# Optimization experiments

Hardware: AMD Instinct MI355X
Metric: run time of the kernel (lower is better)

Reference implementation:

```python
import jax, jax.numpy as jnp
import numpy as np

D = 1024      # input_dim = clip_model.text_projection.shape[1]
P = D // 8    # pre_dim1 == pre_dim2 == 128
B, NS, NT, C = 4096, 8192, 8192, 1000
EPS = 1e-5
SCALE = 0.1
BETA_S = 1.0
BETA_T = 1.0


def setup_inputs() -> dict:
    key = jax.random.key(0)
    ks = jax.random.split(key, 24)
    rn = lambda k, shp, s=0.02: jax.random.normal(k, shp, dtype=jnp.float32) * s
    inp = {
        "Ft": jax.random.normal(ks[0], (C, D), dtype=jnp.float32),
        "Fv": jax.random.normal(ks[1], (B, D), dtype=jnp.float32),
        "Fvs_bank": jax.random.normal(ks[2], (NS, D), dtype=jnp.float32),
        "Fvt_bank": jax.random.normal(ks[3], (NT, D), dtype=jnp.float32),
        # pre_project: Linear(D->P), BN(P), ReLU, Linear(P->P), BN(P), ReLU, Linear(P->3D)
        "W1": rn(ks[4], (P, D)), "b1": jnp.zeros((P,), jnp.float32),
        "g1": jnp.ones((P,), jnp.float32), "be1": jnp.zeros((P,), jnp.float32),
        "m1": jnp.zeros((P,), jnp.float32), "v1": jnp.ones((P,), jnp.float32),
        "W2": rn(ks[5], (P, P)), "b2": jnp.zeros((P,), jnp.float32),
        "g2": jnp.ones((P,), jnp.float32), "be2": jnp.zeros((P,), jnp.float32),
        "m2": jnp.zeros((P,), jnp.float32), "v2": jnp.ones((P,), jnp.float32),
        "W3": rn(ks[6], (3 * D, P)), "b3": jnp.zeros((3 * D,), jnp.float32),
        # post_project: Linear(D->D)
        "Wp": rn(ks[7], (D, D)), "bp": jnp.zeros((D,), jnp.float32),
        "logit_scale": jnp.asarray(np.log(1.0 / 0.07), dtype=jnp.float32),
    }
    return inp


def _pre_project(x, W1, b1, g1, be1, m1, v1, W2, b2, g2, be2, m2, v2, W3, b3):
    # Linear -> BatchNorm1d (eval: running stats) -> ReLU, twice, then Linear to 3*D
    h = x @ W1.T + b1
    h = jax.nn.relu((h - m1) * jax.lax.rsqrt(v1 + EPS) * g1 + be1)
    h = h @ W2.T + b2
    h = jax.nn.relu((h - m2) * jax.lax.rsqrt(v2 + EPS) * g2 + be2)
    return h @ W3.T + b3  # (n, 3*D)


def _qkv(o):
    # einops 'b (d k) -> k b d' with k=3: interleaved split along last dim
    o = o.reshape(o.shape[0], D, 3)
    return o[..., 0], o[..., 1], o[..., 2]


def reference(Ft, Fv, Fvs_bank, Fvt_bank, W1, b1, g1, be1, m1, v1,
              W2, b2, g2, be2, m2, v2, W3, b3, Wp, bp, logit_scale):
    pre = lambda x: _pre_project(x, W1, b1, g1, be1, m1, v1,
                                 W2, b2, g2, be2, m2, v2, W3, b3)
    q_fv, _, _ = _qkv(pre(Fv))
    _, k_fvs, v_fvs = _qkv(pre(Fvs_bank))
    _, k_fvt, v_fvt = _qkv(pre(Fvt_bank))

    As = jax.nn.softmax(SCALE * (q_fv @ k_fvs.T), axis=-1)  # (B, NS)
    At = jax.nn.softmax(SCALE * (q_fv @ k_fvt.T), axis=-1)  # (B, NT)

    Fsa = Fv + (As @ v_fvs) @ Wp.T + bp
    Fta = Fv + (At @ v_fvt) @ Wp.T + bp
    Fsa = Fsa / jnp.linalg.norm(Fsa, axis=-1, keepdims=True)
    Fta = Fta / jnp.linalg.norm(Fta, axis=-1, keepdims=True)

    ls = jnp.exp(logit_scale)
    logits = BETA_S * ls * (Fsa @ Ft.T) + BETA_T * ls * (Fta @ Ft.T)
    return logits  # (B, C)
```

## Files before the change

kernel.cpp:

```cpp
#include <hip/hip_runtime.h>
#include <hip/hip_bf16.h>
#include <math.h>

#define D_DIM   1024
#define P_DIM   128
#define B_ROWS  4096
#define NBANK   8192
#define C_CLS   1000
#define EPS_BN  1e-5f
#define SCALE_S 0.1f
#define MTOT    20480
#define KVSEG   16
#define KCH     64
#define CHUNKS  (NBANK / KVSEG / KCH)

typedef __bf16 bf16x8 __attribute__((ext_vector_type(8)));
typedef float  f32x4  __attribute__((ext_vector_type(4)));
typedef __hip_bfloat16 bf;

__device__ __forceinline__ void load_lds16(const void* gp, void* lp) {
    __builtin_amdgcn_global_load_lds(
        (__attribute__((address_space(1))) void*)gp,
        (__attribute__((address_space(3))) void*)lp, 16, 0, 0);
}

__device__ __forceinline__ int4 pack8(float4 a, float4 b) {
    union { bf h[8]; int4 v; } u;
    u.h[0] = __float2bfloat16(a.x); u.h[1] = __float2bfloat16(a.y);
    u.h[2] = __float2bfloat16(a.z); u.h[3] = __float2bfloat16(a.w);
    u.h[4] = __float2bfloat16(b.x); u.h[5] = __float2bfloat16(b.y);
    u.h[6] = __float2bfloat16(b.z); u.h[7] = __float2bfloat16(b.w);
    return u.v;
}

__global__ __launch_bounds__(256)
void gemm_bf16(const bf* __restrict__ A, const bf* __restrict__ B,
               int M, int N, int K, int lda, int ldb,
               int kchunks, int fx, int fy, int epi,
               float* __restrict__ Cf, bf* __restrict__ Cb,
               const float* __restrict__ bias, const float* __restrict__ biasm,
               const float* __restrict__ bng, const float* __restrict__ bnb,
               const float* __restrict__ bnm, const float* __restrict__ bnv,
               const float* __restrict__ addsrc, const float* __restrict__ lsp,
               int ldc)
{
    __shared__ __align__(16) short ldsS[8192];
    short* lsA = ldsS;
    short* lsB = ldsS + 4096;

    const int tid  = threadIdx.x;
    const int wave = tid >> 6;
    const int lane = tid & 63;
    const int wm   = wave >> 1;
    const int wn   = wave & 1;
    const int r16  = lane & 15;
    const int quad = lane >> 4;

    const int gx = gridDim.x, gy = gridDim.y;
    const int l   = blockIdx.y * gx + blockIdx.x;
    const int xcd = l & 7;
    const int i0  = l >> 3;
    const int sx  = gx / fx, sy = gy / fy;
    const int bx  = (xcd % fx) * sx + (i0 % sx);
    const int by  = (xcd / fx) * sy + (i0 / sx);
    const int bm0 = by * 128;
    const int bn0 = bx * 128;

    const int kper = K / kchunks;
    const int kbeg = blockIdx.z * kper;
    const int kend = kbeg + kper;

    f32x4 acc[4][4];
#pragma unroll
    for (int i = 0; i < 4; ++i)
#pragma unroll
        for (int j = 0; j < 4; ++j) acc[i][j] = (f32x4){0.f, 0.f, 0.f, 0.f};

    for (int k0 = kbeg; k0 < kend; k0 += 32) {
#pragma unroll
        for (int i = 0; i < 2; ++i) {
            const int s   = i * 256 + tid;
            const int row = s >> 2;
            const int cc  = (s & 3) * 8;
            const int lofs = (i * 256 + wave * 64) * 16;
            load_lds16(A + (size_t)(bm0 + row) * lda + k0 + cc, (char*)lsA + lofs);
            load_lds16(B + (size_t)(bn0 + row) * ldb + k0 + cc, (char*)lsB + lofs);
        }
        __syncthreads();

        bf16x8 af[4], bfr[4];
#pragma unroll
        for (int i = 0; i < 4; ++i)
            af[i] = *(const bf16x8*)(lsA + (wm * 64 + i * 16 + r16) * 32 + quad * 8);
#pragma unroll
        for (int j = 0; j < 4; ++j)
            bfr[j] = *(const bf16x8*)(lsB + (wn * 64 + j * 16 + r16) * 32 + quad * 8);
#pragma unroll
        for (int i = 0; i < 4; ++i)
#pragma unroll
            for (int j = 0; j < 4; ++j)
                acc[i][j] = __builtin_amdgcn_mfma_f32_16x16x32_bf16(
                    af[i], bfr[j], acc[i][j], 0, 0, 0);
        __syncthreads();
    }

    if (epi == 3 || epi == 4) {
        const float lsv = (epi == 4) ? expf(*lsp) : 1.0f;
#pragma unroll
        for (int i = 0; i < 4; ++i) {
            const int gmb = bm0 + wm * 64 + i * 16 + quad * 4;
#pragma unroll
            for (int j = 0; j < 4; ++j) {
                const int gn = bn0 + wn * 64 + j * 16 + r16;
#pragma unroll
                for (int r = 0; r < 4; ++r) {
                    const int gm = gmb + r;
                    float val = acc[i][j][r];
                    if (epi == 3) {
                        Cf[(size_t)gm * N + gn] =
                            val + bias[gn] + addsrc[(size_t)(gm & (ldc - 1)) * N + gn];
                    } else {
                        if (gn < ldc) Cf[(size_t)gm * ldc + gn] = val * lsv;
                    }
                }
            }
        }
        return;
    }

    bf* dst = Cb + (epi == 6 ? (size_t)blockIdx.z * M * N : 0);
    bf* my  = (bf*)(ldsS + wave * 2048);

#pragma unroll
    for (int half = 0; half < 2; ++half) {
#pragma unroll
        for (int i2 = 0; i2 < 2; ++i2) {
            const int i = half * 2 + i2;
            const int gmb = bm0 + wm * 64 + i * 16 + quad * 4;
#pragma unroll
            for (int j = 0; j < 4; ++j) {
                const int gn = bn0 + wn * 64 + j * 16 + r16;
#pragma unroll
                for (int r = 0; r < 4; ++r) {
                    float val = acc[i][j][r];
                    if (epi == 1) {
                        val += bias[gn];
                        val = (val - bnm[gn]) * rsqrtf(bnv[gn] + EPS_BN) * bng[gn] + bnb[gn];
                        val = fmaxf(val, 0.f);
                    } else {
                        if (bias)  val += bias[gn];
                        if (biasm) val += biasm[gmb + r];
                    }
                    my[(i2 * 16 + quad * 4 + r) * 64 + j * 16 + r16] =
                        __float2bfloat16(val);
                }
            }
        }
#pragma unroll
        for (int it = 0; it < 4; ++it) {
            const int chunk = it * 64 + lane;
            const int lrow  = chunk >> 3;
            const int lcol  = (chunk & 7) * 8;
            const int grow  = bm0 + wm * 64 + half * 32 + lrow;
            const int gcol  = bn0 + wn * 64 + lcol;
            int4 v = *(const int4*)(my + lrow * 64 + lcol);
            *(int4*)(dst + (size_t)grow * N + gcol) = v;
        }
    }
}

__global__ __launch_bounds__(512)
void attn_fused(const bf* __restrict__ qt,
                const bf* __restrict__ h2bank,
                const bf* __restrict__ h2T,
                const float* __restrict__ beta,
                bf* __restrict__ Ypart,
                float* __restrict__ rsP)
{
    __shared__ __align__(16) short lds[24576];
    short* lsK = lds;
    short* lsV = lds + 8192;
    short* lsS = lds + 16384;

    const int tid  = threadIdx.x;
    const int wave = tid >> 6;
    const int lane = tid & 63;
    const int r16  = lane & 15;
    const int quad = lane >> 4;

    const int qb   = blockIdx.x >> 5;
    const int side = (blockIdx.x >> 4) & 1;
    const int seg  = blockIdx.x & 15;
    const int part = side * KVSEG + seg;
    const int nseg0 = seg * (NBANK / KVSEG);
    const bf* kbase = h2bank + (size_t)side * NBANK * P_DIM;
    const int ncol0 = side * NBANK;

    const bf* qrow = qt + (size_t)(qb * 128 + wave * 16 + r16) * P_DIM;
    bf16x8 qreg[4];
#pragma unroll
    for (int ks = 0; ks < 4; ++ks)
        qreg[ks] = *(const bf16x8*)(qrow + (ks * 4 + quad) * 8);

    f32x4 yacc[8];
    float rsacc[4] = {0.f, 0.f, 0.f, 0.f};
#pragma unroll
    for (int j = 0; j < 8; ++j) yacc[j] = (f32x4){0.f, 0.f, 0.f, 0.f};

    for (int c = 0; c < CHUNKS; ++c) {
        const int kv0 = nseg0 + c * KCH;
        __syncthreads();
#pragma unroll
        for (int m = 0; m < 2; ++m) {
            const int s = m * 512 + tid;
            const int row = s >> 4, pcg = s & 15;
            const int lcg = pcg ^ (row & 15);
            load_lds16(kbase + (size_t)(kv0 + row) * P_DIM + lcg * 8,
                       (char*)lsK + (m * 512 + wave * 64) * 16);
        }
#pragma unroll
        for (int m = 0; m < 2; ++m) {
            const int s = m * 512 + tid;
            const int row = s >> 3, pcg = s & 7;
            const int lcg = pcg ^ (row & 7);
            load_lds16(h2T + (size_t)row * (2 * NBANK) + ncol0 + kv0 + lcg * 8,
                       (char*)lsV + (m * 512 + wave * 64) * 16);
        }
        __syncthreads();

        f32x4 sacc[4];
#pragma unroll
        for (int j = 0; j < 4; ++j) sacc[j] = (f32x4){0.f, 0.f, 0.f, 0.f};
#pragma unroll
        for (int ks = 0; ks < 4; ++ks) {
            bf16x8 bfr[4];
#pragma unroll
            for (int j = 0; j < 4; ++j) {
                const int kr = j * 16 + r16;
                bfr[j] = *(const bf16x8*)(lsK + kr * 128 +
                                          ((ks * 4 + quad) ^ (kr & 15)) * 8);
            }
#pragma unroll
            for (int j = 0; j < 4; ++j)
                sacc[j] = __builtin_amdgcn_mfma_f32_16x16x32_bf16(
                    qreg[ks], bfr[j], sacc[j], 0, 0, 0);
        }

#pragma unroll
        for (int j = 0; j < 4; ++j) {
            const int col = j * 16 + r16;
            const float bv = beta[(size_t)side * NBANK + kv0 + col];
            const int cg = col >> 3, cl = col & 7;
#pragma unroll
            for (int r = 0; r < 4; ++r) {
                const int row = wave * 16 + quad * 4 + r;
                float v = __expf(SCALE_S * (sacc[j][r] + bv));
                rsacc[r] += v;
                ((bf*)lsS)[row * 64 + ((cg ^ (row & 7)) << 3) + cl] =
                    __float2bfloat16(v);
            }
        }

#pragma unroll
        for (int ks = 0; ks < 2; ++ks) {
            const int sr = wave * 16 + r16;
            bf16x8 pa = *(const bf16x8*)(lsS + sr * 64 +
                                         ((ks * 4 + quad) ^ (sr & 7)) * 8);
            bf16x8 pb[8];
#pragma unroll
            for (int j = 0; j < 8; ++j) {
                const int vr = j * 16 + r16;
                pb[j] = *(const bf16x8*)(lsV + vr * 64 +
                                         ((ks * 4 + quad) ^ (vr & 7)) * 8);
            }
#pragma unroll
            for (int j = 0; j < 8; ++j)
                yacc[j] = __builtin_amdgcn_mfma_f32_16x16x32_bf16(
                    pa, pb[j], yacc[j], 0, 0, 0);
        }
    }

#pragma unroll
    for (int r = 0; r < 4; ++r) {
        float s = rsacc[r];
        s += __shfl_xor(s, 1, 64);
        s += __shfl_xor(s, 2, 64);
        s += __shfl_xor(s, 4, 64);
        s += __shfl_xor(s, 8, 64);
        rsacc[r] = s;
    }
    if (r16 == 0)
        *(float4*)(rsP + (size_t)part * B_ROWS + qb * 128 + wave * 16 + quad * 4) =
            (float4){rsacc[0], rsacc[1], rsacc[2], rsacc[3]};

    __syncthreads();
    bf* my = (bf*)lds + wave * 2048;
#pragma unroll
    for (int j = 0; j < 8; ++j)
#pragma unroll
        for (int r = 0; r < 4; ++r)
            my[(quad * 4 + r) * 128 + j * 16 + r16] =
                __float2bfloat16(yacc[j][r]);
    bf* dst = Ypart + (size_t)part * B_ROWS * P_DIM
                    + (size_t)(qb * 128 + wave * 16) * P_DIM;
#pragma unroll
    for (int it = 0; it < 4; ++it) {
        const int chunk = it * 64 + lane;
        const int lrow  = chunk >> 4;
        const int lcol  = (chunk & 15) * 8;
        *(int4*)(dst + (size_t)lrow * P_DIM + lcol) =
            *(const int4*)(my + lrow * 128 + lcol);
    }
}

#define PG0 10240
#define PG1 584
#define PG2 64
#define PG3 512
#define PG4 8
#define PG5 256

__global__ __launch_bounds__(256)
void prep(const float* __restrict__ Fv, const float* __restrict__ Fvs,
          const float* __restrict__ Fvt,
          const float* __restrict__ W1, const float* __restrict__ W2,
          const float* __restrict__ Wp,
          const float* __restrict__ W3, const float* __restrict__ b3,
          const float* __restrict__ bp, const float* __restrict__ Ft,
          bf* __restrict__ Xb, bf* __restrict__ W1b, bf* __restrict__ W2b,
          bf* __restrict__ Wpb,
          bf* __restrict__ Tq, bf* __restrict__ Tk, bf* __restrict__ Tv,
          bf* __restrict__ Ftb,
          float* __restrict__ vvecP, float* __restrict__ bvp)
{
    const int tid = threadIdx.x;
    int b = blockIdx.x;
    if (b < PG0) {
        int i = (b * 256 + tid) * 8;
        const int n0 = B_ROWS * D_DIM, n1 = n0 + NBANK * D_DIM;
        const float* src; int off;
        if (i < n0)      { src = Fv;  off = i; }
        else if (i < n1) { src = Fvs; off = i - n0; }
        else             { src = Fvt; off = i - n1; }
        float4 a = *(const float4*)(src + off);
        float4 c = *(const float4*)(src + off + 4);
        *(int4*)(Xb + i) = pack8(a, c);
        return;
    }
    if ((b -= PG0) < PG1) {
        int i = (b * 256 + tid) * 8;
        const int n1 = P_DIM * D_DIM, n2 = n1 + P_DIM * P_DIM;
        const float* src; bf* dst; int off;
        if (i < n1)      { src = W1; dst = W1b; off = i; }
        else if (i < n2) { src = W2; dst = W2b; off = i - n1; }
        else             { src = Wp; dst = Wpb; off = i - n2; }
        float4 a = *(const float4*)(src + off);
        float4 c = *(const float4*)(src + off + 4);
        *(int4*)(dst + off) = pack8(a, c);
        return;
    }
    if ((b -= PG1) < PG2) {
        int i = (b * 256 + tid) * 8;
        int p = i >> 10, d0 = i & 1023;
        union { bf h[8]; int4 v; } uq, uk, uv;
#pragma unroll
        for (int j = 0; j < 8; ++j) {
            const float* r = W3 + (size_t)3 * (d0 + j) * P_DIM + p;
            uq.h[j] = __float2bfloat16(r[0]);
            uk.h[j] = __float2bfloat16(r[P_DIM]);
            uv.h[j] = __float2bfloat16(r[2 * P_DIM]);
        }
        *(int4*)(Tq + i) = uq.v;
        *(int4*)(Tk + i) = uk.v;
        *(int4*)(Tv + i) = uv.v;
        return;
    }
    if ((b -= PG2) < PG3) {
        int i = (b * 256 + tid) * 8;
        int row = i >> 10, col = i & 1023;
        if (row < C_CLS) {
            float4 a = *(const float4*)(Ft + (size_t)row * D_DIM + col);
            float4 c = *(const float4*)(Ft + (size_t)row * D_DIM + col + 4);
            *(int4*)(Ftb + i) = pack8(a, c);
        } else {
            *(int4*)(Ftb + i) = (int4){0, 0, 0, 0};
        }
        return;
    }
    if ((b -= PG3) < PG4) {
        const int p = tid & 127, hf = tid >> 7;
        const int dbase = b * 128 + hf * 64;
        float s = 0.f;
        for (int dd = 0; dd < 64; ++dd) {
            const int d = dbase + dd;
            s = fmaf(b3[3 * d], W3[(size_t)(3 * d + 1) * P_DIM + p], s);
        }
        vvecP[(b * 2 + hf) * P_DIM + p] = s;
        return;
    }
    b -= PG4;
    const int wave = tid >> 6, lane = tid & 63;
    const int o = b * 4 + wave;
    const float* r = Wp + (size_t)o * D_DIM;
    float s = 0.f;
    for (int i = lane; i < D_DIM; i += 64) s = fmaf(r[i], b3[3 * i + 2], s);
    for (int off = 32; off > 0; off >>= 1) s += __shfl_down(s, off, 64);
    if (lane == 0) bvp[o] = s + bp[o];
}

__global__ __launch_bounds__(256)
void reduceWW(const bf* __restrict__ WqkP, const bf* __restrict__ WpvP,
              bf* __restrict__ Wqk, bf* __restrict__ Wpv)
{
    const int tid = threadIdx.x;
    if (blockIdx.x < 8) {
        int i = (blockIdx.x * 256 + tid) * 8;
        float s[8] = {};
        for (int z = 0; z < 8; ++z) {
            union { int4 v; bf h[8]; } u;
            u.v = *(const int4*)(WqkP + (size_t)z * 16384 + i);
#pragma unroll
            for (int e = 0; e < 8; ++e) s[e] += __bfloat162float(u.h[e]);
        }
        union { bf h[8]; int4 v; } o;
#pragma unroll
        for (int e = 0; e < 8; ++e) o.h[e] = __float2bfloat16(s[e]);
        *(int4*)(Wqk + i) = o.v;
    } else {
        int i = ((blockIdx.x - 8) * 256 + tid) * 8;
        float s[8] = {};
        for (int z = 0; z < 4; ++z) {
            union { int4 v; bf h[8]; } u;
            u.v = *(const int4*)(WpvP + (size_t)z * 131072 + i);
#pragma unroll
            for (int e = 0; e < 8; ++e) s[e] += __bfloat162float(u.h[e]);
        }
        union { bf h[8]; int4 v; } o;
#pragma unroll
        for (int e = 0; e < 8; ++e) o.h[e] = __float2bfloat16(s[e]);
        *(int4*)(Wpv + i) = o.v;
    }
}

__global__ __launch_bounds__(256)
void posth2(const bf* __restrict__ h2bank, const float* __restrict__ vvecP,
            float* __restrict__ beta, bf* __restrict__ h2T)
{
    __shared__ float vs[P_DIM];
    __shared__ bf t[64][136];
    const int tid = threadIdx.x;
    if (blockIdx.x < 64) {
        if (tid < P_DIM) {
            float s = 0.f;
#pragma unroll
            for (int z = 0; z < 16; ++z) s += vvecP[z * P_DIM + tid];
            vs[tid] = s;
        }
        __syncthreads();
        const int n = blockIdx.x * 256 + tid;
        const bf* r = h2bank + (size_t)n * P_DIM;
        float s = 0.f;
#pragma unroll
        for (int c = 0; c < P_DIM; c += 8) {
            union { int4 q; bf h[8]; } u;
            u.q = *(const int4*)(r + c);
#pragma unroll
            for (int e = 0; e < 8; ++e) s += __bfloat162float(u.h[e]) * vs[c + e];
        }
        beta[n] = s;
    } else {
        const size_t n0 = (size_t)(blockIdx.x - 64) * 64;
#pragma unroll
        for (int q = 0; q < 4; ++q) {
            int idx = (q * 256 + tid) * 8;
            int r = idx >> 7, c = idx & 127;
            *(int4*)&t[r][c] = *(const int4*)(h2bank + (n0 + r) * P_DIM + c);
        }
        __syncthreads();
        const int p  = tid >> 1;
        const int nb = (tid & 1) * 32;
#pragma unroll
        for (int q = 0; q < 4; ++q) {
            const int n = nb + q * 8;
            union { int4 v; bf h[8]; } u;
#pragma unroll
            for (int e = 0; e < 8; ++e) u.h[e] = t[n + e][p];
            *(int4*)(h2T + (size_t)p * (2 * NBANK) + n0 + n) = u.v;
        }
    }
}

__global__ __launch_bounds__(256)
void reduceY(const bf* __restrict__ parts, const float* __restrict__ rsP,
             bf* __restrict__ Yhat)
{
    int j = (blockIdx.x * 256 + threadIdx.x) * 8;
    const int s = j >> 19;
    const int qrow = (j >> 7) & (B_ROWS - 1);
    float rs = 0.f;
#pragma unroll
    for (int g = 0; g < KVSEG; ++g)
        rs += rsP[(size_t)(s * KVSEG + g) * B_ROWS + qrow];
    const bf* p = parts + (size_t)s * KVSEG * 524288 + (size_t)(j & 524287);
    float acc[8] = {};
    for (int z = 0; z < KVSEG; ++z) {
        union { int4 v; bf h[8]; } u;
        u.v = *(const int4*)(p + (size_t)z * 524288);
#pragma unroll
        for (int e = 0; e < 8; ++e) acc[e] += __bfloat162float(u.h[e]);
    }
    const float inv = 1.0f / rs;
    union { bf h[8]; int4 v; } o;
#pragma unroll
    for (int e = 0; e < 8; ++e) o.h[e] = __float2bfloat16(acc[e] * inv);
    *(int4*)(Yhat + j) = o.v;
}

__global__ __launch_bounds__(256)
void rownorm2b(const float* __restrict__ G, bf* __restrict__ out)
{
    __shared__ float red[16];
    const int tid = threadIdx.x;
    const float* ps = G + (size_t)blockIdx.x * D_DIM;
    const float* pt = ps + (size_t)B_ROWS * D_DIM;
    float4 a = *(const float4*)(ps + tid * 4);
    float4 c = *(const float4*)(pt + tid * 4);
    float sa = a.x * a.x + a.y * a.y + a.z * a.z + a.w * a.w;
    float sb = c.x * c.x + c.y * c.y + c.z * c.z + c.w * c.w;
    for (int s = 32; s > 0; s >>= 1) {
        sa += __shfl_down(sa, s, 64);
        sb += __shfl_down(sb, s, 64);
    }
    if ((tid & 63) == 0) { red[tid >> 6] = sa; red[8 + (tid >> 6)] = sb; }
    __syncthreads();
    if (tid == 0) {
        float ta = 0.f, tb = 0.f;
        for (int w = 0; w < 4; ++w) { ta += red[w]; tb += red[8 + w]; }
        red[4] = rsqrtf(ta); red[12] = rsqrtf(tb);
    }
    __syncthreads();
    const float ia = red[4], ib = red[12];
    union { bf h[4]; int2 v; } o;
    o.h[0] = __float2bfloat16(a.x * ia + c.x * ib);
    o.h[1] = __float2bfloat16(a.y * ia + c.y * ib);
    o.h[2] = __float2bfloat16(a.z * ia + c.z * ib);
    o.h[3] = __float2bfloat16(a.w * ia + c.w * ib);
    *(int2*)(out + (size_t)blockIdx.x * D_DIM + tid * 4) = o.v;
}

extern "C" void kernel_launch(void* const* d_in, const int* in_sizes, int n_in,
                              void* d_out, int out_size, void* d_ws, size_t ws_size,
                              hipStream_t stream)
{
    (void)in_sizes; (void)n_in; (void)out_size; (void)ws_size;

    const float* Ft  = (const float*)d_in[0];
    const float* Fv  = (const float*)d_in[1];
    const float* Fvs = (const float*)d_in[2];
    const float* Fvt = (const float*)d_in[3];
    const float* W1  = (const float*)d_in[4];
    const float* b1  = (const float*)d_in[5];
    const float* g1  = (const float*)d_in[6];
    const float* be1 = (const float*)d_in[7];
    const float* m1  = (const float*)d_in[8];
    const float* v1  = (const float*)d_in[9];
    const float* W2  = (const float*)d_in[10];
    const float* b2  = (const float*)d_in[11];
    const float* g2  = (const float*)d_in[12];
    const float* be2 = (const float*)d_in[13];
    const float* m2  = (const float*)d_in[14];
    const float* v2  = (const float*)d_in[15];
    const float* W3  = (const float*)d_in[16];
    const float* b3  = (const float*)d_in[17];
    const float* Wp  = (const float*)d_in[18];
    const float* bp  = (const float*)d_in[19];
    const float* ls  = (const float*)d_in[20];

    char* base = (char*)d_ws;
    size_t o = 0;
    auto take = [&](size_t s) { size_t r = o; o += (s + 255) & ~(size_t)255; return r; };

    bf* qtb   = (bf*)(base + take((size_t)B_ROWS * P_DIM * 2));
    bf* h2T   = (bf*)(base + take((size_t)P_DIM * 2 * NBANK * 2));
    bf* Yhat  = (bf*)(base + take((size_t)2 * B_ROWS * P_DIM * 2));
    bf* Wpb   = (bf*)(base + take((size_t)D_DIM * D_DIM * 2));
    bf* Ftb   = (bf*)(base + take((size_t)D_DIM * D_DIM * 2));
    bf* W3qT  = (bf*)(base + take((size_t)P_DIM * D_DIM * 2));
    bf* W3kT  = (bf*)(base + take((size_t)P_DIM * D_DIM * 2));
    bf* W3vT  = (bf*)(base + take((size_t)P_DIM * D_DIM * 2));
    bf* Wqk   = (bf*)(base + take((size_t)P_DIM * P_DIM * 2));
    bf* Wpvb  = (bf*)(base + take((size_t)D_DIM * P_DIM * 2));
    bf* W1b   = (bf*)(base + take((size_t)P_DIM * D_DIM * 2));
    bf* W2b   = (bf*)(base + take((size_t)P_DIM * P_DIM * 2));
    bf* h2b   = (bf*)(base + take((size_t)MTOT * P_DIM * 2));
    bf* WqkP  = (bf*)(base + take((size_t)8 * P_DIM * P_DIM * 2));
    bf* WpvP  = (bf*)(base + take((size_t)4 * D_DIM * P_DIM * 2));
    float* vvecP = (float*)(base + take((size_t)16 * P_DIM * 4));
    float* beta  = (float*)(base + take((size_t)2 * NBANK * 4));
    float* bvp   = (float*)(base + take(D_DIM * 4));
    float* rsP   = (float*)(base + take((size_t)2 * KVSEG * B_ROWS * 4));

    const size_t Dbase = o;
    bf* Xb    = (bf*)(base + Dbase);
    bf* h1b   = (bf*)(base + Dbase + (size_t)MTOT * D_DIM * 2);
    bf* Opart = (bf*)(base + Dbase + (size_t)48 * 1024 * 1024);
    float* G     = (float*)(base + Dbase);
    bf*    Fsumb = (bf*)(base + Dbase + (size_t)2 * B_ROWS * D_DIM * 4);

    auto gemm = [&](const bf* A, const bf* B, int M, int N, int K, int lda, int ldb,
                    int kch, int fx, int fy, int epi, float* Cf, bf* Cb,
                    const float* bias, const float* biasm,
                    const float* bg, const float* bb, const float* bm, const float* bv,
                    const float* addsrc, const float* lsp, int ldc) {
        gemm_bf16<<<dim3(N / 128, M / 128, kch), dim3(256), 0, stream>>>(
            A, B, M, N, K, lda, ldb, kch, fx, fy, epi, Cf, Cb, bias, biasm,
            bg, bb, bm, bv, addsrc, lsp, ldc);
    };

    prep<<<dim3(PG0 + PG1 + PG2 + PG3 + PG4 + PG5), dim3(256), 0, stream>>>(
        Fv, Fvs, Fvt, W1, W2, Wp, W3, b3, bp, Ft,
        Xb, W1b, W2b, Wpb, W3qT, W3kT, W3vT, Ftb, vvecP, bvp);

    gemm(W3kT, W3qT, P_DIM, P_DIM, D_DIM, D_DIM, D_DIM, 8, 1, 1, 6, nullptr, WqkP,
         nullptr, nullptr, nullptr, nullptr, nullptr, nullptr, nullptr, nullptr, 0);
    gemm(Wpb, W3vT, D_DIM, P_DIM, D_DIM, D_DIM, D_DIM, 4, 1, 8, 6, nullptr, WpvP,
         nullptr, nullptr, nullptr, nullptr, nullptr, nullptr, nullptr, nullptr, 0);
    reduceWW<<<dim3(72), dim3(256), 0, stream>>>(WqkP, WpvP, Wqk, Wpvb);

    gemm(Xb, W1b, MTOT, P_DIM, D_DIM, D_DIM, D_DIM, 1, 1, 8, 1, nullptr, h1b,
         b1, nullptr, g1, be1, m1, v1, nullptr, nullptr, 0);
    gemm(h1b, W2b, MTOT, P_DIM, P_DIM, P_DIM, P_DIM, 1, 1, 8, 1, nullptr, h2b,
         b2, nullptr, g2, be2, m2, v2, nullptr, nullptr, 0);
    gemm(h2b, Wqk, B_ROWS, P_DIM, P_DIM, P_DIM, P_DIM, 1, 1, 8, 5, nullptr, qtb,
         nullptr, nullptr, nullptr, nullptr, nullptr, nullptr, nullptr, nullptr, 0);
    posth2<<<dim3(320), dim3(256), 0, stream>>>(
        h2b + (size_t)B_ROWS * P_DIM, vvecP, beta, h2T);

    attn_fused<<<dim3(2 * KVSEG * (B_ROWS / 128)), dim3(512), 0, stream>>>(
        qtb, h2b + (size_t)B_ROWS * P_DIM, h2T, beta, Opart, rsP);
    reduceY<<<dim3(2 * B_ROWS * P_DIM / 2048), dim3(256), 0, stream>>>(
        Opart, rsP, Yhat);

    gemm(Yhat, Wpvb, 2 * B_ROWS, D_DIM, P_DIM, P_DIM, P_DIM, 1, 1, 8, 3, G, nullptr,
         bvp, nullptr, nullptr, nullptr, nullptr, nullptr, Fv, nullptr, B_ROWS);
    rownorm2b<<<dim3(B_ROWS), dim3(256), 0, stream>>>(G, Fsumb);
    gemm(Fsumb, Ftb, B_ROWS, D_DIM, D_DIM, D_DIM, D_DIM, 1, 1, 8, 4, (float*)d_out,
         nullptr, nullptr, nullptr, nullptr, nullptr, nullptr, nullptr, nullptr,
         ls, C_CLS);
}
```

Measured before the change: 373.7 us.

## Split-K first projection GEMM and fuse BN/ReLU, second layer and q projection

The first Linear(D->P) GEMM over all 20480 rows now runs with split-K of 2 and writes raw fp32 partials. A new h2fuse kernel sums the partials, applies the folded BN1 affine and ReLU, runs the 128x128 second layer with BN2/ReLU, and for query rows also computes the q projection, all from LDS. This removes two GEMM launches and the h1 round trip through memory, and doubles the grid of the large GEMM (only 160 row tiles before). In exchange it writes fp32 partials (20 MB) instead of bf16 h1, and adds a small BN folding block to prep.

```diff
diff --git a/kernel.cpp b/kernel.cpp
--- a/kernel.cpp
+++ b/kernel.cpp
@@ -104,6 +104,22 @@
         __syncthreads();
     }
 
+    if (epi == 8) {
+        float* dst = Cf + (size_t)blockIdx.z * M * N;
+#pragma unroll
+        for (int i = 0; i < 4; ++i) {
+            const int gmb = bm0 + wm * 64 + i * 16 + quad * 4;
+#pragma unroll
+            for (int j = 0; j < 4; ++j) {
+                const int gn = bn0 + wn * 64 + j * 16 + r16;
+#pragma unroll
+                for (int r = 0; r < 4; ++r)
+                    dst[(size_t)(gmb + r) * N + gn] = acc[i][j][r];
+            }
+        }
+        return;
+    }
+
     if (epi == 3 || epi == 4) {
         const float lsv = (epi == 4) ? expf(*lsp) : 1.0f;
 #pragma unroll
@@ -169,6 +185,177 @@
     }
 }
 
+__global__ __launch_bounds__(256)
+void h2fuse(const float* __restrict__ Hp,
+            const bf* __restrict__ W2b,
+            const bf* __restrict__ Wqk,
+            const float* __restrict__ bnA,
+            bf* __restrict__ h2b, bf* __restrict__ qtb)
+{
+    __shared__ __align__(16) short lsH[16384];
+    __shared__ __align__(16) short lsW[16384];
+    __shared__ float sA1[128], sC1[128], sA2[128], sC2[128];
+
+    const int tid  = threadIdx.x;
+    const int wave = tid >> 6;
+    const int lane = tid & 63;
+    const int r16  = lane & 15;
+    const int quad = lane >> 4;
+    const int wm   = wave >> 1;
+    const int wn   = wave & 1;
+    const int r0   = blockIdx.x * 128;
+    const bool isq = (r0 < B_ROWS);
+
+#pragma unroll
+    for (int m = 0; m < 8; ++m) {
+        const int s = m * 256 + tid;
+        const int row = s >> 4, pcg = s & 15;
+        load_lds16(W2b + row * 128 + (pcg ^ (row & 15)) * 8,
+                   (char*)lsW + (m * 256 + wave * 64) * 16);
+    }
+    if (tid < 128) {
+        sA1[tid] = bnA[tid];       sC1[tid] = bnA[128 + tid];
+        sA2[tid] = bnA[256 + tid]; sC2[tid] = bnA[384 + tid];
+    }
+    __syncthreads();
+
+#pragma unroll
+    for (int m = 0; m < 16; ++m) {
+        const int s = m * 256 + tid;
+        const int row = s >> 5;
+        const int col = (s & 31) * 4;
+        const float* p0 = Hp + (size_t)(r0 + row) * 128 + col;
+        float4 x0 = *(const float4*)p0;
+        float4 x1 = *(const float4*)(p0 + (size_t)MTOT * 128);
+        union { bf h[4]; int2 v; } u;
+        u.h[0] = __float2bfloat16(fmaxf(fmaf(x0.x + x1.x, sA1[col],     sC1[col]),     0.f));
+        u.h[1] = __float2bfloat16(fmaxf(fmaf(x0.y + x1.y, sA1[col + 1], sC1[col + 1]), 0.f));
+        u.h[2] = __float2bfloat16(fmaxf(fmaf(x0.z + x1.z, sA1[col + 2], sC1[col + 2]), 0.f));
+        u.h[3] = __float2bfloat16(fmaxf(fmaf(x0.w + x1.w, sA1[col + 3], sC1[col + 3]), 0.f));
+        const int cg = col >> 3;
+        *(int2*)((bf*)lsH + row * 128 + ((cg ^ (row & 15)) << 3) + (col & 7)) = u.v;
+    }
+    __syncthreads();
+
+    f32x4 acc[4][4];
+#pragma unroll
+    for (int i = 0; i < 4; ++i)
+#pragma unroll
+        for (int j = 0; j < 4; ++j) acc[i][j] = (f32x4){0.f, 0.f, 0.f, 0.f};
+#pragma unroll
+    for (int ks = 0; ks < 4; ++ks) {
+        bf16x8 af[4], bfr[4];
+#pragma unroll
+        for (int i = 0; i < 4; ++i) {
+            const int row = wm * 64 + i * 16 + r16;
+            af[i] = *(const bf16x8*)(lsH + row * 128 + ((ks * 4 + quad) ^ (row & 15)) * 8);
+        }
+#pragma unroll
+        for (int j = 0; j < 4; ++j) {
+            const int row = wn * 64 + j * 16 + r16;
+            bfr[j] = *(const bf16x8*)(lsW + row * 128 + ((ks * 4 + quad) ^ (row & 15)) * 8);
+        }
+#pragma unroll
+        for (int i = 0; i < 4; ++i)
+#pragma unroll
+            for (int j = 0; j < 4; ++j)
+                acc[i][j] = __builtin_amdgcn_mfma_f32_16x16x32_bf16(
+                    af[i], bfr[j], acc[i][j], 0, 0, 0);
+    }
+    __syncthreads();
+
+    if (isq) {
+#pragma unroll
+        for (int m = 0; m < 8; ++m) {
+            const int s = m * 256 + tid;
+            const int row = s >> 4, pcg = s & 15;
+            load_lds16(Wqk + row * 128 + (pcg ^ (row & 15)) * 8,
+                       (char*)lsW + (m * 256 + wave * 64) * 16);
+        }
+    }
+
+#pragma unroll
+    for (int i = 0; i < 4; ++i) {
+#pragma unroll
+        for (int j = 0; j < 4; ++j) {
+            const int gn = wn * 64 + j * 16 + r16;
+            const int cg = gn >> 3, cl = gn & 7;
+            const float a2 = sA2[gn], c2 = sC2[gn];
+#pragma unroll
+            for (int r = 0; r < 4; ++r) {
+                const int row = wm * 64 + i * 16 + quad * 4 + r;
+                float v = fmaxf(fmaf(acc[i][j][r], a2, c2), 0.f);
+                ((bf*)lsH)[row * 128 + ((cg ^ (row & 15)) << 3) + cl] =
+                    __float2bfloat16(v);
+            }
+        }
+    }
+    __syncthreads();
+
+#pragma unroll
+    for (int m = 0; m < 8; ++m) {
+        const int s = m * 256 + tid;
+        const int row = s >> 4, cg = s & 15;
+        *(int4*)(h2b + (size_t)(r0 + row) * 128 + cg * 8) =
+            *(const int4*)(lsH + row * 128 + ((cg ^ (row & 15)) << 3));
+    }
+
+    if (!isq) return;
+
+    f32x4 acc2[4][4];
+#pragma unroll
+    for (int i = 0; i < 4; ++i)
+#pragma unroll
+        for (int j = 0; j < 4; ++j) acc2[i][j] = (f32x4){0.f, 0.f, 0.f, 0.f};
+#pragma unroll
+    for (int ks = 0; ks < 4; ++ks) {
+        bf16x8 af[4], bfr[4];
+#pragma unroll
+        for (int i = 0; i < 4; ++i) {
+            const int row = wm * 64 + i * 16 + r16;
+            af[i] = *(const bf16x8*)(lsH + row * 128 + ((ks * 4 + quad) ^ (row & 15)) * 8);
+        }
+#pragma unroll
+        for (int j = 0; j < 4; ++j) {
+            const int row = wn * 64 + j * 16 + r16;
+            bfr[j] = *(const bf16x8*)(lsW + row * 128 + ((ks * 4 + quad) ^ (row & 15)) * 8);
+        }
+#pragma unroll
+        for (int i = 0; i < 4; ++i)
+#pragma unroll
+            for (int j = 0; j < 4; ++j)
+                acc2[i][j] = __builtin_amdgcn_mfma_f32_16x16x32_bf16(
+                    af[i], bfr[j], acc2[i][j], 0, 0, 0);
+    }
+    __syncthreads();
+
+    bf* my  = (bf*)lsW + wave * 2048;
+    bf* dst = qtb + (size_t)r0 * 128;
+#pragma unroll
+    for (int half = 0; half < 2; ++half) {
+#pragma unroll
+        for (int i2 = 0; i2 < 2; ++i2) {
+            const int i = half * 2 + i2;
+#pragma unroll
+            for (int j = 0; j < 4; ++j)
+#pragma unroll
+                for (int r = 0; r < 4; ++r)
+                    my[(i2 * 16 + quad * 4 + r) * 64 + j * 16 + r16] =
+                        __float2bfloat16(acc2[i][j][r]);
+        }
+#pragma unroll
+        for (int it = 0; it < 4; ++it) {
+            const int chunk = it * 64 + lane;
+            const int lrow  = chunk >> 3;
+            const int lcol  = (chunk & 7) * 8;
+            const int grow  = wm * 64 + half * 32 + lrow;
+            const int gcol  = wn * 64 + lcol;
+            int4 v = *(const int4*)(my + lrow * 64 + lcol);
+            *(int4*)(dst + (size_t)grow * 128 + gcol) = v;
+        }
+    }
+}
+
 __global__ __launch_bounds__(512)
 void attn_fused(const bf* __restrict__ qt,
                 const bf* __restrict__ h2bank,
@@ -319,6 +506,7 @@
 #define PG3 512
 #define PG4 8
 #define PG5 256
+#define PG6 1
 
 __global__ __launch_bounds__(256)
 void prep(const float* __restrict__ Fv, const float* __restrict__ Fvs,
@@ -327,11 +515,18 @@
           const float* __restrict__ Wp,
           const float* __restrict__ W3, const float* __restrict__ b3,
           const float* __restrict__ bp, const float* __restrict__ Ft,
+          const float* __restrict__ b1, const float* __restrict__ g1,
+          const float* __restrict__ be1, const float* __restrict__ m1,
+          const float* __restrict__ v1,
+          const float* __restrict__ b2, const float* __restrict__ g2,
+          const float* __restrict__ be2, const float* __restrict__ m2,
+          const float* __restrict__ v2,
           bf* __restrict__ Xb, bf* __restrict__ W1b, bf* __restrict__ W2b,
           bf* __restrict__ Wpb,
           bf* __restrict__ Tq, bf* __restrict__ Tk, bf* __restrict__ Tv,
           bf* __restrict__ Ftb,
-          float* __restrict__ vvecP, float* __restrict__ bvp)
+          float* __restrict__ vvecP, float* __restrict__ bvp,
+          float* __restrict__ bnA)
 {
     const int tid = threadIdx.x;
     int b = blockIdx.x;
@@ -398,14 +593,24 @@
         vvecP[(b * 2 + hf) * P_DIM + p] = s;
         return;
     }
-    b -= PG4;
-    const int wave = tid >> 6, lane = tid & 63;
-    const int o = b * 4 + wave;
-    const float* r = Wp + (size_t)o * D_DIM;
-    float s = 0.f;
-    for (int i = lane; i < D_DIM; i += 64) s = fmaf(r[i], b3[3 * i + 2], s);
-    for (int off = 32; off > 0; off >>= 1) s += __shfl_down(s, off, 64);
-    if (lane == 0) bvp[o] = s + bp[o];
+    if ((b -= PG4) < PG5) {
+        const int wave = tid >> 6, lane = tid & 63;
+        const int o = b * 4 + wave;
+        const float* r = Wp + (size_t)o * D_DIM;
+        float s = 0.f;
+        for (int i = lane; i < D_DIM; i += 64) s = fmaf(r[i], b3[3 * i + 2], s);
+        for (int off = 32; off > 0; off >>= 1) s += __shfl_down(s, off, 64);
+        if (lane == 0) bvp[o] = s + bp[o];
+        return;
+    }
+    if (tid < 128) {
+        float a1 = g1[tid] * rsqrtf(v1[tid] + EPS_BN);
+        bnA[tid]       = a1;
+        bnA[128 + tid] = (b1[tid] - m1[tid]) * a1 + be1[tid];
+        float a2 = g2[tid] * rsqrtf(v2[tid] + EPS_BN);
+        bnA[256 + tid] = a2;
+        bnA[384 + tid] = (b2[tid] - m2[tid]) * a2 + be2[tid];
+    }
 }
 
 __global__ __launch_bounds__(256)
@@ -598,12 +803,13 @@
     float* vvecP = (float*)(base + take((size_t)16 * P_DIM * 4));
     float* beta  = (float*)(base + take((size_t)2 * NBANK * 4));
     float* bvp   = (float*)(base + take(D_DIM * 4));
+    float* bnA   = (float*)(base + take(4 * P_DIM * 4));
     float* rsP   = (float*)(base + take((size_t)2 * KVSEG * B_ROWS * 4));
 
     const size_t Dbase = o;
-    bf* Xb    = (bf*)(base + Dbase);
-    bf* h1b   = (bf*)(base + Dbase + (size_t)MTOT * D_DIM * 2);
-    bf* Opart = (bf*)(base + Dbase + (size_t)48 * 1024 * 1024);
+    bf*    Xb    = (bf*)(base + Dbase);
+    float* Hp    = (float*)(base + Dbase + (size_t)MTOT * D_DIM * 2);
+    bf*    Opart = (bf*)(base + Dbase + (size_t)64 * 1024 * 1024);
     float* G     = (float*)(base + Dbase);
     bf*    Fsumb = (bf*)(base + Dbase + (size_t)2 * B_ROWS * D_DIM * 4);
 
@@ -617,9 +823,10 @@
             bg, bb, bm, bv, addsrc, lsp, ldc);
     };
 
-    prep<<<dim3(PG0 + PG1 + PG2 + PG3 + PG4 + PG5), dim3(256), 0, stream>>>(
+    prep<<<dim3(PG0 + PG1 + PG2 + PG3 + PG4 + PG5 + PG6), dim3(256), 0, stream>>>(
         Fv, Fvs, Fvt, W1, W2, Wp, W3, b3, bp, Ft,
-        Xb, W1b, W2b, Wpb, W3qT, W3kT, W3vT, Ftb, vvecP, bvp);
+        b1, g1, be1, m1, v1, b2, g2, be2, m2, v2,
+        Xb, W1b, W2b, Wpb, W3qT, W3kT, W3vT, Ftb, vvecP, bvp, bnA);
 
     gemm(W3kT, W3qT, P_DIM, P_DIM, D_DIM, D_DIM, D_DIM, 8, 1, 1, 6, nullptr, WqkP,
          nullptr, nullptr, nullptr, nullptr, nullptr, nullptr, nullptr, nullptr, 0);
@@ -627,12 +834,10 @@
          nullptr, nullptr, nullptr, nullptr, nullptr, nullptr, nullptr, nullptr, 0);
     reduceWW<<<dim3(72), dim3(256), 0, stream>>>(WqkP, WpvP, Wqk, Wpvb);
 
-    gemm(Xb, W1b, MTOT, P_DIM, D_DIM, D_DIM, D_DIM, 1, 1, 8, 1, nullptr, h1b,
-         b1, nullptr, g1, be1, m1, v1, nullptr, nullptr, 0);
-    gemm(h1b, W2b, MTOT, P_DIM, P_DIM, P_DIM, P_DIM, 1, 1, 8, 1, nullptr, h2b,
-         b2, nullptr, g2, be2, m2, v2, nullptr, nullptr, 0);
-    gemm(h2b, Wqk, B_ROWS, P_DIM, P_DIM, P_DIM, P_DIM, 1, 1, 8, 5, nullptr, qtb,
+    gemm(Xb, W1b, MTOT, P_DIM, D_DIM, D_DIM, D_DIM, 2, 1, 8, 8, Hp, nullptr,
          nullptr, nullptr, nullptr, nullptr, nullptr, nullptr, nullptr, nullptr, 0);
+    h2fuse<<<dim3(MTOT / 128), dim3(256), 0, stream>>>(
+        Hp, W2b, Wqk, bnA, h2b, qtb);
     posth2<<<dim3(320), dim3(256), 0, stream>>>(
         h2b + (size_t)B_ROWS * P_DIM, vvecP, beta, h2T);
 
```

After: 348.5 us. -6.7%, faster.
